# Kernel tuning notes

Hardware: AMD Instinct MI355X
Metric: run time of the kernel (lower is better)

Reference implementation:

```python
import jax, jax.numpy as jnp
import numpy as np

N_NODES = 10000
N_EDGES = 320000
IN_F, H1, H2 = 512, 256, 64


def setup_inputs() -> dict:
    key = jax.random.key(0)
    ks = jax.random.split(key, 8)
    x = jax.random.normal(ks[0], (N_NODES, IN_F), dtype=jnp.float32)
    edge_src = jax.random.randint(ks[1], (N_EDGES,), 0, N_NODES, dtype=jnp.int32)
    edge_dst = jax.random.randint(ks[2], (N_EDGES,), 0, N_NODES, dtype=jnp.int32)
    edge_weight = jax.random.uniform(ks[3], (N_EDGES,), dtype=jnp.float32)
    # Glorot-initialized GCN weights + biases
    W1 = jax.random.normal(ks[4], (IN_F, H1), dtype=jnp.float32) * (1.0 / np.sqrt(IN_F))
    b1 = jnp.zeros((H1,), dtype=jnp.float32)
    W2 = jax.random.normal(ks[5], (H1, H2), dtype=jnp.float32) * (1.0 / np.sqrt(H1))
    b2 = jnp.zeros((H2,), dtype=jnp.float32)
    return {"x": x, "W1": W1, "b1": b1, "W2": W2, "b2": b2,
            "edge_weight": edge_weight, "edge_src": edge_src, "edge_dst": edge_dst}


def _gcn_layer(h, W, b, edge_src, edge_dst, edge_weight, act):
    # support = h @ W  (dropout is identity in eval mode)
    support = h @ W  # [N, out]
    # sparse adjacency aggregation: out[dst] += w * support[src]
    msgs = support[edge_src] * edge_weight[:, None]  # [E, out]
    agg = jax.ops.segment_sum(msgs, edge_dst, num_segments=h.shape[0])
    return act(agg + b)


def reference(x, W1, b1, W2, b2, edge_weight, edge_src, edge_dst):
    h1 = _gcn_layer(x, W1, b1, edge_src, edge_dst, edge_weight, jax.nn.relu)
    z = _gcn_layer(h1, W2, b2, edge_src, edge_dst, edge_weight, jax.nn.relu)  # embeddings
    # InnerProductDecoder: sigmoid(z @ z.T)
    recon = jax.nn.sigmoid(z @ z.T)  # [N, N]
    return (z, recon)
```

## Files before the change

### kernel.cpp

```cpp
#include <hip/hip_runtime.h>

#define N_NODES 10000
#define N_EDGES 320000
#define IN_F    512
#define H1F     256
#define H2F     64

typedef __attribute__((ext_vector_type(8)))  short short8;
typedef __attribute__((ext_vector_type(16))) float f32x16;

__device__ __forceinline__ unsigned short f2bf(float f) {
    union { float fl; unsigned int i; } v; v.fl = f;
    unsigned int x = v.i;
    return (unsigned short)((x + 0x7fffu + ((x >> 16) & 1u)) >> 16);
}
__device__ __forceinline__ float bf2f(unsigned short u) {
    union { unsigned int i; float f; } v; v.i = ((unsigned int)u) << 16; return v.f;
}

__device__ __forceinline__ bool edge_is_alpha(int a0) {
    return (unsigned)a0 < N_NODES;
}

__global__ __launch_bounds__(256) void k_hist(const int* __restrict__ c0,
                                              const int* __restrict__ c2,
                                              int* __restrict__ deg) {
    int e = blockIdx.x * 256 + threadIdx.x;
    if (e >= N_EDGES) return;
    int a0 = c0[e];
    int dst = edge_is_alpha(a0) ? a0 : c2[e];
    if ((unsigned)dst < N_NODES) atomicAdd(&deg[dst], 1);
}

__global__ __launch_bounds__(1024) void k_scan(const int* __restrict__ deg,
                                               int* __restrict__ off,
                                               int* __restrict__ cursor) {
    __shared__ int part[1024];
    int t = threadIdx.x;
    const int chunk = (N_NODES + 1023) / 1024;
    int begin = t * chunk;
    int end = begin + chunk; if (end > N_NODES) end = N_NODES;
    if (begin > N_NODES) begin = N_NODES;
    int s = 0;
    for (int i = begin; i < end; ++i) s += deg[i];
    part[t] = s;
    __syncthreads();
    for (int o = 1; o < 1024; o <<= 1) {
        int v = (t >= o) ? part[t - o] : 0;
        __syncthreads();
        part[t] += v;
        __syncthreads();
    }
    int base = (t == 0) ? 0 : part[t - 1];
    for (int i = begin; i < end; ++i) {
        off[i] = base; cursor[i] = base; base += deg[i];
    }
    if (t == 1023) off[N_NODES] = part[1023];
}

__global__ __launch_bounds__(256) void k_bucket(const int* __restrict__ c0,
                                                const int* __restrict__ c1,
                                                const int* __restrict__ c2,
                                                const float* __restrict__ c0f,
                                                const float* __restrict__ c2f,
                                                int* __restrict__ cursor,
                                                int2* __restrict__ ep) {
    int e = blockIdx.x * 256 + threadIdx.x;
    if (e >= N_EDGES) return;
    int a0 = c0[e];
    bool alpha = edge_is_alpha(a0);
    int src = c1[e];
    int dst = alpha ? a0 : c2[e];
    float w = alpha ? c2f[e] : c0f[e];
    if ((unsigned)src >= N_NODES || (unsigned)dst >= N_NODES) return;
    int p = atomicAdd(&cursor[dst], 1);
    ep[p] = make_int2(src, __float_as_int(w));
}

__global__ __launch_bounds__(256) void k_gemm1(const float* __restrict__ x,
                                               const float* __restrict__ W1,
                                               unsigned short* __restrict__ sup1b) {
    __shared__ float xs[IN_F][8];
    int nb = blockIdx.x * 8;
    int t = threadIdx.x;
    {
        int n  = t & 7;
        int k0 = (t >> 3) * 16;
        const float* xr = x + (size_t)(nb + n) * IN_F + k0;
        #pragma unroll
        for (int c = 0; c < 16; c += 4) {
            float4 v = *(const float4*)(xr + c);
            xs[k0 + c + 0][n] = v.x;
            xs[k0 + c + 1][n] = v.y;
            xs[k0 + c + 2][n] = v.z;
            xs[k0 + c + 3][n] = v.w;
        }
    }
    __syncthreads();
    int f = t;
    float acc[8] = {0.f,0.f,0.f,0.f,0.f,0.f,0.f,0.f};
    #pragma unroll 8
    for (int k = 0; k < IN_F; ++k) {
        float w = W1[(size_t)k * H1F + f];
        float4 a = *(const float4*)&xs[k][0];
        float4 b = *(const float4*)&xs[k][4];
        acc[0] += a.x * w; acc[1] += a.y * w; acc[2] += a.z * w; acc[3] += a.w * w;
        acc[4] += b.x * w; acc[5] += b.y * w; acc[6] += b.z * w; acc[7] += b.w * w;
    }
    #pragma unroll
    for (int n = 0; n < 8; ++n)
        sup1b[(size_t)(nb + n) * H1F + f] = f2bf(acc[n]);
}

__global__ __launch_bounds__(256) void k_agg1(const unsigned short* __restrict__ sup1b,
                                              const int* __restrict__ off,
                                              const int2* __restrict__ ep,
                                              const float* __restrict__ b1,
                                              float* __restrict__ h1) {
    __shared__ int2 eds[256];
    int node = blockIdx.x;
    int f = threadIdx.x;
    int s = off[node], e = off[node + 1];
    float a0 = 0.f, a1 = 0.f, a2 = 0.f, a3 = 0.f;
    for (int base = s; base < e; base += 256) {
        int n = e - base; if (n > 256) n = 256;
        __syncthreads();
        if (f < n) eds[f] = ep[base + f];
        __syncthreads();
        int j = 0;
        for (; j + 4 <= n; j += 4) {
            int2 e0 = eds[j], e1 = eds[j+1], e2 = eds[j+2], e3 = eds[j+3];
            a0 += __int_as_float(e0.y) * bf2f(sup1b[(size_t)e0.x * H1F + f]);
            a1 += __int_as_float(e1.y) * bf2f(sup1b[(size_t)e1.x * H1F + f]);
            a2 += __int_as_float(e2.y) * bf2f(sup1b[(size_t)e2.x * H1F + f]);
            a3 += __int_as_float(e3.y) * bf2f(sup1b[(size_t)e3.x * H1F + f]);
        }
        for (; j < n; ++j) {
            int2 e0 = eds[j];
            a0 += __int_as_float(e0.y) * bf2f(sup1b[(size_t)e0.x * H1F + f]);
        }
    }
    float acc = (a0 + a1) + (a2 + a3);
    h1[(size_t)node * H1F + f] = fmaxf(acc + b1[f], 0.f);
}

__global__ __launch_bounds__(64) void k_gemm2(const float* __restrict__ h1,
                                              const float* __restrict__ W2,
                                              float* __restrict__ sup2) {
    __shared__ float hs[H1F][4];
    int nb = blockIdx.x * 4;
    int t = threadIdx.x;
    {
        int n  = t & 3;
        int k0 = (t >> 2) * 16;
        const float* hr = h1 + (size_t)(nb + n) * H1F + k0;
        #pragma unroll
        for (int c = 0; c < 16; c += 4) {
            float4 v = *(const float4*)(hr + c);
            hs[k0 + c + 0][n] = v.x;
            hs[k0 + c + 1][n] = v.y;
            hs[k0 + c + 2][n] = v.z;
            hs[k0 + c + 3][n] = v.w;
        }
    }
    __syncthreads();
    int f = t;
    float acc[4] = {0.f,0.f,0.f,0.f};
    #pragma unroll 8
    for (int k = 0; k < H1F; ++k) {
        float w = W2[(size_t)k * H2F + f];
        float4 a = *(const float4*)&hs[k][0];
        acc[0] += a.x * w; acc[1] += a.y * w; acc[2] += a.z * w; acc[3] += a.w * w;
    }
    #pragma unroll
    for (int n = 0; n < 4; ++n)
        sup2[(size_t)(nb + n) * H2F + f] = acc[n];
}

__global__ __launch_bounds__(64) void k_agg2(const float* __restrict__ sup2,
                                             const int* __restrict__ off,
                                             const int2* __restrict__ ep,
                                             const float* __restrict__ b2,
                                             float* __restrict__ zout,
                                             unsigned short* __restrict__ zb) {
    __shared__ int2 eds[64];
    int node = blockIdx.x;
    int f = threadIdx.x;
    int s = off[node], e = off[node + 1];
    float a0 = 0.f, a1 = 0.f, a2 = 0.f, a3 = 0.f;
    for (int base = s; base < e; base += 64) {
        int n = e - base; if (n > 64) n = 64;
        __syncthreads();
        if (f < n) eds[f] = ep[base + f];
        __syncthreads();
        int j = 0;
        for (; j + 4 <= n; j += 4) {
            int2 e0 = eds[j], e1 = eds[j+1], e2 = eds[j+2], e3 = eds[j+3];
            a0 += __int_as_float(e0.y) * sup2[(size_t)e0.x * H2F + f];
            a1 += __int_as_float(e1.y) * sup2[(size_t)e1.x * H2F + f];
            a2 += __int_as_float(e2.y) * sup2[(size_t)e2.x * H2F + f];
            a3 += __int_as_float(e3.y) * sup2[(size_t)e3.x * H2F + f];
        }
        for (; j < n; ++j) {
            int2 e0 = eds[j];
            a0 += __int_as_float(e0.y) * sup2[(size_t)e0.x * H2F + f];
        }
    }
    float acc = (a0 + a1) + (a2 + a3);
    acc = fmaxf(acc + b2[f], 0.f);
    zout[(size_t)node * H2F + f] = acc;
    zb[(size_t)node * H2F + f] = f2bf(acc);
}

__global__ __launch_bounds__(256) void k_decoder(const unsigned short* __restrict__ zb,
                                                 float* __restrict__ recon) {
    int t = threadIdx.x;
    int wave = t >> 6, lane = t & 63;
    int i0 = blockIdx.y * 64 + (wave >> 1) * 32;
    int j0 = blockIdx.x * 64 + (wave & 1) * 32;
    int r = lane & 31, half = lane >> 5;
    int arow = i0 + r, brow = j0 + r;

    short8 zero8 = {0,0,0,0,0,0,0,0};
    short8 a[4], b[4];
    #pragma unroll
    for (int s = 0; s < 4; ++s) {
        a[s] = (arow < N_NODES) ? *(const short8*)(zb + (size_t)arow * H2F + s * 16 + half * 8)
                                : zero8;
        b[s] = (brow < N_NODES) ? *(const short8*)(zb + (size_t)brow * H2F + s * 16 + half * 8)
                                : zero8;
    }

    f32x16 acc;
    #pragma unroll
    for (int i = 0; i < 16; ++i) acc[i] = 0.f;
    #pragma unroll
    for (int s = 0; s < 4; ++s)
        acc = __builtin_amdgcn_mfma_f32_32x32x16_bf16(a[s], b[s], acc, 0, 0, 0);

    #pragma unroll
    for (int rg = 0; rg < 16; ++rg) {
        int row = i0 + (rg & 3) + 8 * (rg >> 2) + 4 * half;
        int col = j0 + r;
        if (row < N_NODES && col < N_NODES) {
            float sv = acc[rg];
            recon[(size_t)row * N_NODES + col] = 1.0f / (1.0f + __expf(-sv));
        }
    }
}

extern "C" void kernel_launch(void* const* d_in, const int* in_sizes, int n_in,
                              void* d_out, int out_size, void* d_ws, size_t ws_size,
                              hipStream_t stream) {
    int ix = -1, iW1 = -1, ib1 = -1, iW2 = -1, ib2 = -1, ic0 = -1, ic1 = -1, ic2 = -1;
    for (int i = 0; i < n_in; ++i) {
        int s = in_sizes[i];
        if      (s == N_NODES * IN_F) ix = i;
        else if (s == IN_F * H1F)     iW1 = i;
        else if (s == H1F)            ib1 = i;
        else if (s == H1F * H2F)      iW2 = i;
        else if (s == H2F)            ib2 = i;
        else if (s == N_EDGES) { if (ic0 < 0) ic0 = i; else if (ic1 < 0) ic1 = i; else ic2 = i; }
    }
    if (ix < 0 || iW1 < 0 || ib1 < 0 || iW2 < 0 || ib2 < 0 || ic0 < 0 || ic1 < 0 || ic2 < 0) {
        ix = 0; iW1 = 1; ib1 = 2; iW2 = 3; ib2 = 4; ic0 = 5; ic1 = 6; ic2 = 7;
    }
    const float* x  = (const float*)d_in[ix];
    const float* W1 = (const float*)d_in[iW1];
    const float* b1 = (const float*)d_in[ib1];
    const float* W2 = (const float*)d_in[iW2];
    const float* b2 = (const float*)d_in[ib2];
    const int*   c0  = (const int*)d_in[ic0];
    const int*   c1  = (const int*)d_in[ic1];
    const int*   c2  = (const int*)d_in[ic2];
    const float* c0f = (const float*)d_in[ic0];
    const float* c2f = (const float*)d_in[ic2];

    float* zout  = (float*)d_out;
    float* recon = zout + (size_t)N_NODES * H2F;

    unsigned short* zb = (unsigned short*)d_ws;

    char* scratch = (char*)recon;
    size_t o = 0;
    auto alloc = [&](size_t bytes) { size_t p = o; o += (bytes + 255) & ~(size_t)255; return p; };
    int*            deg    = (int*)           (scratch + alloc((size_t)N_NODES * 4));
    int*            off    = (int*)           (scratch + alloc((size_t)(N_NODES + 1) * 4));
    int*            cursor = (int*)           (scratch + alloc((size_t)N_NODES * 4));
    int2*           ep     = (int2*)          (scratch + alloc((size_t)N_EDGES * 8));
    unsigned short* sup1b  = (unsigned short*)(scratch + alloc((size_t)N_NODES * H1F * 2));
    float*          h1     = (float*)         (scratch + alloc((size_t)N_NODES * H1F * 4));
    float*          sup2   = (float*)         (scratch + alloc((size_t)N_NODES * H2F * 4));

    hipMemsetAsync(deg, 0, (size_t)N_NODES * 4, stream);
    k_hist  <<<(N_EDGES + 255) / 256, 256, 0, stream>>>(c0, c2, deg);
    k_scan  <<<1, 1024, 0, stream>>>(deg, off, cursor);
    k_bucket<<<(N_EDGES + 255) / 256, 256, 0, stream>>>(c0, c1, c2, c0f, c2f, cursor, ep);

    k_gemm1<<<N_NODES / 8, 256, 0, stream>>>(x, W1, sup1b);
    k_agg1 <<<N_NODES, 256, 0, stream>>>(sup1b, off, ep, b1, h1);

    k_gemm2<<<N_NODES / 4, 64, 0, stream>>>(h1, W2, sup2);
    k_agg2 <<<N_NODES, 64, 0, stream>>>(sup2, off, ep, b2, zout, zb);

    dim3 dgrid((N_NODES + 63) / 64, (N_NODES + 63) / 64);
    k_decoder<<<dgrid, 256, 0, stream>>>(zb, recon);
}
```

Measured before the change: 611.6 us.

## Use bf16 MFMA for both GEMMs and fuse CSR build into cooperative kernel

Replaces the scalar FP32 GEMMs for both GCN layers with bf16 MFMA 32x32x16 kernels, reading pre-transposed bf16 weights produced by a new transpose kernel. Merges the histogram, scan and bucket kernels plus the memset into one cooperative kernel that uses grid syncs. The aim is to cut FP32 ALU time in the GEMMs and the launch overhead of the CSR build. In exchange, inputs are rounded to bf16 before the matmuls, which loses precision, and the CSR work now runs on only 256 blocks with grid-wide barriers.

```diff
diff --git a/kernel.cpp b/kernel.cpp
--- a/kernel.cpp
+++ b/kernel.cpp
@@ -1,4 +1,6 @@
 #include <hip/hip_runtime.h>
+#include <hip/hip_cooperative_groups.h>
+namespace cg = cooperative_groups;
 
 #define N_NODES 10000
 #define N_EDGES 320000
@@ -17,99 +19,179 @@
 __device__ __forceinline__ float bf2f(unsigned short u) {
     union { unsigned int i; float f; } v; v.i = ((unsigned int)u) << 16; return v.f;
 }
-
 __device__ __forceinline__ bool edge_is_alpha(int a0) {
     return (unsigned)a0 < N_NODES;
 }
 
-__global__ __launch_bounds__(256) void k_hist(const int* __restrict__ c0,
-                                              const int* __restrict__ c2,
-                                              int* __restrict__ deg) {
-    int e = blockIdx.x * 256 + threadIdx.x;
-    if (e >= N_EDGES) return;
-    int a0 = c0[e];
-    int dst = edge_is_alpha(a0) ? a0 : c2[e];
-    if ((unsigned)dst < N_NODES) atomicAdd(&deg[dst], 1);
-}
-
-__global__ __launch_bounds__(1024) void k_scan(const int* __restrict__ deg,
-                                               int* __restrict__ off,
-                                               int* __restrict__ cursor) {
-    __shared__ int part[1024];
+__global__ void k_csr(const int* __restrict__ c0, const int* __restrict__ c1,
+                      const int* __restrict__ c2, const float* __restrict__ c0f,
+                      const float* __restrict__ c2f,
+                      int* __restrict__ deg, int* __restrict__ off,
+                      int* __restrict__ cursor, int2* __restrict__ ep,
+                      int* __restrict__ partial, int* __restrict__ pex) {
+    cg::grid_group grid = cg::this_grid();
+    int b = blockIdx.x, t = threadIdx.x;
+    int gtid = b * 256 + t, gsz = gridDim.x * 256;
+    __shared__ int incl[64];
+    const int CH = 40;
+    for (int i = gtid; i < N_NODES; i += gsz) deg[i] = 0;
+    grid.sync();
+    for (int e = gtid; e < N_EDGES; e += gsz) {
+        int a0 = c0[e];
+        int dst = edge_is_alpha(a0) ? a0 : c2[e];
+        if ((unsigned)dst < N_NODES) atomicAdd(&deg[dst], 1);
+    }
+    grid.sync();
+    if (t < 64) {
+        int i = b * CH + t;
+        int v = (t < CH && i < N_NODES) ? deg[i] : 0;
+        #pragma unroll
+        for (int o2 = 1; o2 < 64; o2 <<= 1) {
+            int u = __shfl_up(v, o2, 64);
+            if (t >= o2) v += u;
+        }
+        incl[t] = v;
+        if (t == 63) partial[b] = v;
+    }
+    grid.sync();
+    if (b == 0 && t < 64) {
+        int i4 = t * 4;
+        int p0 = partial[i4], p1 = partial[i4+1], p2 = partial[i4+2], p3 = partial[i4+3];
+        int s0 = p0, s1 = s0 + p1, s2 = s1 + p2, s3 = s2 + p3;
+        int v = s3;
+        #pragma unroll
+        for (int o2 = 1; o2 < 64; o2 <<= 1) {
+            int u = __shfl_up(v, o2, 64);
+            if (t >= o2) v += u;
+        }
+        int ebase = v - s3;
+        pex[i4] = ebase; pex[i4+1] = ebase + s0; pex[i4+2] = ebase + s1; pex[i4+3] = ebase + s2;
+    }
+    grid.sync();
+    if (t < CH) {
+        int i = b * CH + t;
+        if (i < N_NODES) {
+            int val = pex[b] + (t ? incl[t-1] : 0);
+            off[i] = val; cursor[i] = val;
+            if (i == N_NODES - 1) off[N_NODES] = pex[b] + incl[t];
+        }
+    }
+    grid.sync();
+    for (int e = gtid; e < N_EDGES; e += gsz) {
+        int a0 = c0[e];
+        bool alpha = edge_is_alpha(a0);
+        int src = c1[e];
+        int dst = alpha ? a0 : c2[e];
+        float w = alpha ? c2f[e] : c0f[e];
+        if ((unsigned)src >= N_NODES || (unsigned)dst >= N_NODES) continue;
+        int p = atomicAdd(&cursor[dst], 1);
+        ep[p] = make_int2(src, __float_as_int(w));
+    }
+}
+
+__global__ __launch_bounds__(256) void k_wtrans(const float* __restrict__ W1,
+                                                const float* __restrict__ W2,
+                                                unsigned short* __restrict__ W1t,
+                                                unsigned short* __restrict__ W2t) {
+    int idx = blockIdx.x * 256 + threadIdx.x;
+    if (idx < IN_F * H1F) {
+        int k = idx / H1F, f = idx % H1F;
+        W1t[(size_t)f * IN_F + k] = f2bf(W1[idx]);
+    }
+    int idx2 = idx - IN_F * H1F;
+    if (idx2 >= 0 && idx2 < H1F * H2F) {
+        int k = idx2 / H2F, f = idx2 % H2F;
+        W2t[(size_t)f * H1F + k] = f2bf(W2[idx2]);
+    }
+}
+
+__global__ __launch_bounds__(256) void k_gemm1m(const float* __restrict__ x,
+                                                const unsigned short* __restrict__ W1t,
+                                                unsigned short* __restrict__ sup1b) {
+    __shared__ unsigned short As[2 * 64 * 8];
     int t = threadIdx.x;
-    const int chunk = (N_NODES + 1023) / 1024;
-    int begin = t * chunk;
-    int end = begin + chunk; if (end > N_NODES) end = N_NODES;
-    if (begin > N_NODES) begin = N_NODES;
-    int s = 0;
-    for (int i = begin; i < end; ++i) s += deg[i];
-    part[t] = s;
-    __syncthreads();
-    for (int o = 1; o < 1024; o <<= 1) {
-        int v = (t >= o) ? part[t - o] : 0;
-        __syncthreads();
-        part[t] += v;
-        __syncthreads();
-    }
-    int base = (t == 0) ? 0 : part[t - 1];
-    for (int i = begin; i < end; ++i) {
-        off[i] = base; cursor[i] = base; base += deg[i];
-    }
-    if (t == 1023) off[N_NODES] = part[1023];
-}
-
-__global__ __launch_bounds__(256) void k_bucket(const int* __restrict__ c0,
-                                                const int* __restrict__ c1,
-                                                const int* __restrict__ c2,
-                                                const float* __restrict__ c0f,
-                                                const float* __restrict__ c2f,
-                                                int* __restrict__ cursor,
-                                                int2* __restrict__ ep) {
-    int e = blockIdx.x * 256 + threadIdx.x;
-    if (e >= N_EDGES) return;
-    int a0 = c0[e];
-    bool alpha = edge_is_alpha(a0);
-    int src = c1[e];
-    int dst = alpha ? a0 : c2[e];
-    float w = alpha ? c2f[e] : c0f[e];
-    if ((unsigned)src >= N_NODES || (unsigned)dst >= N_NODES) return;
-    int p = atomicAdd(&cursor[dst], 1);
-    ep[p] = make_int2(src, __float_as_int(w));
-}
-
-__global__ __launch_bounds__(256) void k_gemm1(const float* __restrict__ x,
-                                               const float* __restrict__ W1,
-                                               unsigned short* __restrict__ sup1b) {
-    __shared__ float xs[IN_F][8];
-    int nb = blockIdx.x * 8;
+    int nb = blockIdx.x * 64;
+    int wave = t >> 6, lane = t & 63;
+    int half = lane >> 5, r = lane & 31;
+    int fb = wave * 64;
+    int srow = t >> 2, skk = (t & 3) * 4;
+    unsigned short* sdst = &As[(((skk >> 3) * 64 + srow) * 8) + (skk & 7)];
+    const float* xrow = x + (size_t)(nb + srow) * IN_F + skk;
+    bool svalid = (nb + srow) < N_NODES;
+
+    f32x16 acc[2][2];
+    #pragma unroll
+    for (int mi = 0; mi < 2; mi++)
+        #pragma unroll
+        for (int ni = 0; ni < 2; ni++)
+            #pragma unroll
+            for (int i = 0; i < 16; i++) acc[mi][ni][i] = 0.f;
+
+    for (int k0 = 0; k0 < IN_F; k0 += 16) {
+        __syncthreads();
+        float4 v = svalid ? *(const float4*)(xrow + k0) : make_float4(0.f, 0.f, 0.f, 0.f);
+        ushort4 u; u.x = f2bf(v.x); u.y = f2bf(v.y); u.z = f2bf(v.z); u.w = f2bf(v.w);
+        *(ushort4*)sdst = u;
+        __syncthreads();
+        short8 a0 = *(const short8*)&As[(half * 64 + r) * 8];
+        short8 a1 = *(const short8*)&As[(half * 64 + 32 + r) * 8];
+        short8 b0 = *(const short8*)&W1t[(size_t)(fb + r) * IN_F + k0 + half * 8];
+        short8 b1 = *(const short8*)&W1t[(size_t)(fb + 32 + r) * IN_F + k0 + half * 8];
+        acc[0][0] = __builtin_amdgcn_mfma_f32_32x32x16_bf16(a0, b0, acc[0][0], 0, 0, 0);
+        acc[0][1] = __builtin_amdgcn_mfma_f32_32x32x16_bf16(a0, b1, acc[0][1], 0, 0, 0);
+        acc[1][0] = __builtin_amdgcn_mfma_f32_32x32x16_bf16(a1, b0, acc[1][0], 0, 0, 0);
+        acc[1][1] = __builtin_amdgcn_mfma_f32_32x32x16_bf16(a1, b1, acc[1][1], 0, 0, 0);
+    }
+    #pragma unroll
+    for (int mi = 0; mi < 2; mi++) {
+        #pragma unroll
+        for (int rg = 0; rg < 16; rg++) {
+            int row = nb + mi * 32 + (rg & 3) + 8 * (rg >> 2) + 4 * half;
+            if (row < N_NODES) {
+                #pragma unroll
+                for (int ni = 0; ni < 2; ni++) {
+                    int col = fb + ni * 32 + r;
+                    sup1b[(size_t)row * H1F + col] = f2bf(acc[mi][ni][rg]);
+                }
+            }
+        }
+    }
+}
+
+__global__ __launch_bounds__(256) void k_gemm2m(const float* __restrict__ h1,
+                                                const unsigned short* __restrict__ W2t,
+                                                float* __restrict__ sup2) {
+    __shared__ unsigned short As[2 * 64 * 8];
     int t = threadIdx.x;
-    {
-        int n  = t & 7;
-        int k0 = (t >> 3) * 16;
-        const float* xr = x + (size_t)(nb + n) * IN_F + k0;
-        #pragma unroll
-        for (int c = 0; c < 16; c += 4) {
-            float4 v = *(const float4*)(xr + c);
-            xs[k0 + c + 0][n] = v.x;
-            xs[k0 + c + 1][n] = v.y;
-            xs[k0 + c + 2][n] = v.z;
-            xs[k0 + c + 3][n] = v.w;
-        }
-    }
-    __syncthreads();
-    int f = t;
-    float acc[8] = {0.f,0.f,0.f,0.f,0.f,0.f,0.f,0.f};
-    #pragma unroll 8
-    for (int k = 0; k < IN_F; ++k) {
-        float w = W1[(size_t)k * H1F + f];
-        float4 a = *(const float4*)&xs[k][0];
-        float4 b = *(const float4*)&xs[k][4];
-        acc[0] += a.x * w; acc[1] += a.y * w; acc[2] += a.z * w; acc[3] += a.w * w;
-        acc[4] += b.x * w; acc[5] += b.y * w; acc[6] += b.z * w; acc[7] += b.w * w;
-    }
-    #pragma unroll
-    for (int n = 0; n < 8; ++n)
-        sup1b[(size_t)(nb + n) * H1F + f] = f2bf(acc[n]);
+    int nb = blockIdx.x * 64;
+    int wave = t >> 6, lane = t & 63;
+    int half = lane >> 5, r = lane & 31;
+    int mi = wave >> 1, ni = wave & 1;
+    int srow = t >> 2, skk = (t & 3) * 4;
+    unsigned short* sdst = &As[(((skk >> 3) * 64 + srow) * 8) + (skk & 7)];
+    const float* hrow = h1 + (size_t)(nb + srow) * H1F + skk;
+    bool svalid = (nb + srow) < N_NODES;
+
+    f32x16 acc;
+    #pragma unroll
+    for (int i = 0; i < 16; i++) acc[i] = 0.f;
+
+    for (int k0 = 0; k0 < H1F; k0 += 16) {
+        __syncthreads();
+        float4 v = svalid ? *(const float4*)(hrow + k0) : make_float4(0.f, 0.f, 0.f, 0.f);
+        ushort4 u; u.x = f2bf(v.x); u.y = f2bf(v.y); u.z = f2bf(v.z); u.w = f2bf(v.w);
+        *(ushort4*)sdst = u;
+        __syncthreads();
+        short8 a = *(const short8*)&As[(half * 64 + mi * 32 + r) * 8];
+        short8 b = *(const short8*)&W2t[(size_t)(ni * 32 + r) * H1F + k0 + half * 8];
+        acc = __builtin_amdgcn_mfma_f32_32x32x16_bf16(a, b, acc, 0, 0, 0);
+    }
+    #pragma unroll
+    for (int rg = 0; rg < 16; rg++) {
+        int row = nb + mi * 32 + (rg & 3) + 8 * (rg >> 2) + 4 * half;
+        int col = ni * 32 + r;
+        if (row < N_NODES) sup2[(size_t)row * H2F + col] = acc[rg];
+    }
 }
 
 __global__ __launch_bounds__(256) void k_agg1(const unsigned short* __restrict__ sup1b,
@@ -142,39 +224,6 @@
     }
     float acc = (a0 + a1) + (a2 + a3);
     h1[(size_t)node * H1F + f] = fmaxf(acc + b1[f], 0.f);
-}
-
-__global__ __launch_bounds__(64) void k_gemm2(const float* __restrict__ h1,
-                                              const float* __restrict__ W2,
-                                              float* __restrict__ sup2) {
-    __shared__ float hs[H1F][4];
-    int nb = blockIdx.x * 4;
-    int t = threadIdx.x;
-    {
-        int n  = t & 3;
-        int k0 = (t >> 2) * 16;
-        const float* hr = h1 + (size_t)(nb + n) * H1F + k0;
-        #pragma unroll
-        for (int c = 0; c < 16; c += 4) {
-            float4 v = *(const float4*)(hr + c);
-            hs[k0 + c + 0][n] = v.x;
-            hs[k0 + c + 1][n] = v.y;
-            hs[k0 + c + 2][n] = v.z;
-            hs[k0 + c + 3][n] = v.w;
-        }
-    }
-    __syncthreads();
-    int f = t;
-    float acc[4] = {0.f,0.f,0.f,0.f};
-    #pragma unroll 8
-    for (int k = 0; k < H1F; ++k) {
-        float w = W2[(size_t)k * H2F + f];
-        float4 a = *(const float4*)&hs[k][0];
-        acc[0] += a.x * w; acc[1] += a.y * w; acc[2] += a.z * w; acc[3] += a.w * w;
-    }
-    #pragma unroll
-    for (int n = 0; n < 4; ++n)
-        sup2[(size_t)(nb + n) * H2F + f] = acc[n];
 }
 
 __global__ __launch_bounds__(64) void k_agg2(const float* __restrict__ sup2,
@@ -230,7 +279,6 @@
         b[s] = (brow < N_NODES) ? *(const short8*)(zb + (size_t)brow * H2F + s * 16 + half * 8)
                                 : zero8;
     }
-
     f32x16 acc;
     #pragma unroll
     for (int i = 0; i < 16; ++i) acc[i] = 0.f;
@@ -278,30 +326,37 @@
 
     float* zout  = (float*)d_out;
     float* recon = zout + (size_t)N_NODES * H2F;
-
     unsigned short* zb = (unsigned short*)d_ws;
 
     char* scratch = (char*)recon;
     size_t o = 0;
     auto alloc = [&](size_t bytes) { size_t p = o; o += (bytes + 255) & ~(size_t)255; return p; };
-    int*            deg    = (int*)           (scratch + alloc((size_t)N_NODES * 4));
-    int*            off    = (int*)           (scratch + alloc((size_t)(N_NODES + 1) * 4));
-    int*            cursor = (int*)           (scratch + alloc((size_t)N_NODES * 4));
-    int2*           ep     = (int2*)          (scratch + alloc((size_t)N_EDGES * 8));
-    unsigned short* sup1b  = (unsigned short*)(scratch + alloc((size_t)N_NODES * H1F * 2));
-    float*          h1     = (float*)         (scratch + alloc((size_t)N_NODES * H1F * 4));
-    float*          sup2   = (float*)         (scratch + alloc((size_t)N_NODES * H2F * 4));
-
-    hipMemsetAsync(deg, 0, (size_t)N_NODES * 4, stream);
-    k_hist  <<<(N_EDGES + 255) / 256, 256, 0, stream>>>(c0, c2, deg);
-    k_scan  <<<1, 1024, 0, stream>>>(deg, off, cursor);
-    k_bucket<<<(N_EDGES + 255) / 256, 256, 0, stream>>>(c0, c1, c2, c0f, c2f, cursor, ep);
-
-    k_gemm1<<<N_NODES / 8, 256, 0, stream>>>(x, W1, sup1b);
-    k_agg1 <<<N_NODES, 256, 0, stream>>>(sup1b, off, ep, b1, h1);
-
-    k_gemm2<<<N_NODES / 4, 64, 0, stream>>>(h1, W2, sup2);
-    k_agg2 <<<N_NODES, 64, 0, stream>>>(sup2, off, ep, b2, zout, zb);
+    int*            deg     = (int*)           (scratch + alloc((size_t)N_NODES * 4));
+    int*            off     = (int*)           (scratch + alloc((size_t)(N_NODES + 1) * 4));
+    int*            cursor  = (int*)           (scratch + alloc((size_t)N_NODES * 4));
+    int2*           ep      = (int2*)          (scratch + alloc((size_t)N_EDGES * 8));
+    unsigned short* sup1b   = (unsigned short*)(scratch + alloc((size_t)N_NODES * H1F * 2));
+    float*          h1      = (float*)         (scratch + alloc((size_t)N_NODES * H1F * 4));
+    float*          sup2    = (float*)         (scratch + alloc((size_t)N_NODES * H2F * 4));
+    unsigned short* W1t     = (unsigned short*)(scratch + alloc((size_t)IN_F * H1F * 2));
+    unsigned short* W2t     = (unsigned short*)(scratch + alloc((size_t)H1F * H2F * 2));
+    int*            partial = (int*)           (scratch + alloc(1024));
+    int*            pex     = (int*)           (scratch + alloc(1024 + 4));
+
+    k_wtrans<<<(IN_F * H1F + H1F * H2F + 255) / 256, 256, 0, stream>>>(W1, W2, W1t, W2t);
+
+    {
+        void* args[] = { (void*)&c0, (void*)&c1, (void*)&c2, (void*)&c0f, (void*)&c2f,
+                         (void*)&deg, (void*)&off, (void*)&cursor, (void*)&ep,
+                         (void*)&partial, (void*)&pex };
+        hipLaunchCooperativeKernel((const void*)k_csr, dim3(256), dim3(256), args, 0, stream);
+    }
+
+    k_gemm1m<<<(N_NODES + 63) / 64, 256, 0, stream>>>(x, W1t, sup1b);
+    k_agg1  <<<N_NODES, 256, 0, stream>>>(sup1b, off, ep, b1, h1);
+
+    k_gemm2m<<<(N_NODES + 63) / 64, 256, 0, stream>>>(h1, W2t, sup2);
+    k_agg2  <<<N_NODES, 64, 0, stream>>>(sup2, off, ep, b2, zout, zb);
 
     dim3 dgrid((N_NODES + 63) / 64, (N_NODES + 63) / 64);
     k_decoder<<<dgrid, 256, 0, stream>>>(zb, recon);
```

New measurement: 730.0 us. +19.4%, slower.

## Exploit recon symmetry and stage decoder tiles in LDS for vectorized stores

Applied to the files above, without the earlier changes.

The decoder now computes only the upper-triangular 64x64 tiles, since z·zᵀ is symmetric; lower-triangle blocks exit immediately. Each computed tile is staged in padded shared memory and written with float4 stores, and off-diagonal tiles are also written transposed into the mirrored position. This halves the MFMA and sigmoid work and is meant to improve store coalescing on a kernel dominated by writing the 400 MB output. In exchange it adds an LDS round trip, a barrier, strided transposed LDS reads, and unequal work across blocks.

```diff
diff --git a/kernel.cpp b/kernel.cpp
--- a/kernel.cpp
+++ b/kernel.cpp
@@ -17,7 +17,6 @@
 __device__ __forceinline__ float bf2f(unsigned short u) {
     union { unsigned int i; float f; } v; v.i = ((unsigned int)u) << 16; return v.f;
 }
-
 __device__ __forceinline__ bool edge_is_alpha(int a0) {
     return (unsigned)a0 < N_NODES;
 }
@@ -214,10 +213,13 @@
 
 __global__ __launch_bounds__(256) void k_decoder(const unsigned short* __restrict__ zb,
                                                  float* __restrict__ recon) {
+    int bi = blockIdx.y, bj = blockIdx.x;
+    if (bj < bi) return;
+    __shared__ float Cs[64][65];
     int t = threadIdx.x;
     int wave = t >> 6, lane = t & 63;
-    int i0 = blockIdx.y * 64 + (wave >> 1) * 32;
-    int j0 = blockIdx.x * 64 + (wave & 1) * 32;
+    int wi = (wave >> 1) * 32, wj = (wave & 1) * 32;
+    int i0 = bi * 64 + wi, j0 = bj * 64 + wj;
     int r = lane & 31, half = lane >> 5;
     int arow = i0 + r, brow = j0 + r;
 
@@ -230,7 +232,6 @@
         b[s] = (brow < N_NODES) ? *(const short8*)(zb + (size_t)brow * H2F + s * 16 + half * 8)
                                 : zero8;
     }
-
     f32x16 acc;
     #pragma unroll
     for (int i = 0; i < 16; ++i) acc[i] = 0.f;
@@ -240,11 +241,44 @@
 
     #pragma unroll
     for (int rg = 0; rg < 16; ++rg) {
-        int row = i0 + (rg & 3) + 8 * (rg >> 2) + 4 * half;
-        int col = j0 + r;
-        if (row < N_NODES && col < N_NODES) {
-            float sv = acc[rg];
-            recon[(size_t)row * N_NODES + col] = 1.0f / (1.0f + __expf(-sv));
+        int lr = wi + (rg & 3) + 8 * (rg >> 2) + 4 * half;
+        int lc = wj + r;
+        Cs[lr][lc] = 1.0f / (1.0f + __expf(-acc[rg]));
+    }
+    __syncthreads();
+
+    #pragma unroll
+    for (int p = 0; p < 4; ++p) {
+        int e = p * 1024 + t * 4;
+        int lr = e >> 6, lc = e & 63;
+        int grow = bi * 64 + lr, gcol = bj * 64 + lc;
+        if (grow < N_NODES) {
+            float4 v = *(const float4*)&Cs[lr][lc];
+            size_t base = (size_t)grow * N_NODES + gcol;
+            if (gcol + 4 <= N_NODES) *(float4*)&recon[base] = v;
+            else {
+                const float* vp = &v.x;
+                for (int k = 0; k < 4; ++k)
+                    if (gcol + k < N_NODES) recon[base + k] = vp[k];
+            }
+        }
+    }
+    if (bi != bj) {
+        #pragma unroll
+        for (int p = 0; p < 4; ++p) {
+            int e = p * 1024 + t * 4;
+            int lr = e >> 6, lc = e & 63;
+            int grow = bj * 64 + lr, gcol = bi * 64 + lc;
+            if (grow < N_NODES) {
+                float4 v = make_float4(Cs[lc][lr], Cs[lc+1][lr], Cs[lc+2][lr], Cs[lc+3][lr]);
+                size_t base = (size_t)grow * N_NODES + gcol;
+                if (gcol + 4 <= N_NODES) *(float4*)&recon[base] = v;
+                else {
+                    const float* vp = &v.x;
+                    for (int k = 0; k < 4; ++k)
+                        if (gcol + k < N_NODES) recon[base + k] = vp[k];
+                }
+            }
         }
     }
 }
@@ -278,7 +312,6 @@
 
     float* zout  = (float*)d_out;
     float* recon = zout + (size_t)N_NODES * H2F;
-
     unsigned short* zb = (unsigned short*)d_ws;
 
     char* scratch = (char*)recon;
```

Result: no change. 609.1 us (-0.4%).
